# Kernel optimization log

Hardware: AMD Instinct MI355X
Metric: run time of the kernel (lower is better)

The kernel has to match this reference:

```python
import jax, jax.numpy as jnp
import numpy as np

A, D, F = 2048, 64, 12  # atoms, depth, filter_length


def _chemconv(x, conn, bond, filters):
    # x: (A, D); conn: (A, A, F); bond: (A, F, 2); filters: (D, F, D+2)
    # node_connection = conn.transpose(1,2) @ x -> (A, F, D)
    ncon = jnp.einsum('anf,nd->afd', conn, x)
    combined = jnp.concatenate([ncon, bond], axis=2)  # (A, F, D+2)
    # broadcast-multiply by filters then sum over last two dims -> (A, out_depth)
    return jnp.einsum('afc,ofc->ao', combined, filters)


def setup_inputs() -> dict:
    key = jax.random.key(0)
    k1, k2, k3, k4, k5 = jax.random.split(key, 5)
    x = jax.random.normal(k1, (A, D), dtype=jnp.float32)
    conn = jax.random.uniform(k2, (A, A, F), dtype=jnp.float32)
    bond = jax.random.normal(k3, (A, F, 2), dtype=jnp.float32)
    scale = 1.0 / D  # filters.data.normal_() * (1/in_depth)
    f0 = jax.random.normal(k4, (D, F, D + 2), dtype=jnp.float32) * scale
    f1 = jax.random.normal(k5, (D, F, D + 2), dtype=jnp.float32) * scale
    return {
        'node_property_tensor': x,
        'connectivity_tensor': conn,
        'bond_property_tensor': bond,
        'filters0': f0,
        'filters1': f1,
    }


def reference(node_property_tensor, connectivity_tensor, bond_property_tensor, filters0, filters1):
    x = node_property_tensor
    out = x
    for filt in (filters0, filters1):
        # each ChemConv layer is applied twice (same weights), per the torch code
        out = jax.nn.relu(_chemconv(out, connectivity_tensor, bond_property_tensor, filt))
        out = _chemconv(out, connectivity_tensor, bond_property_tensor, filt)
        out = out + x  # residual to the original block input
        out = jax.nn.relu(out)
    return out
```

## Files before the change

kernel.cpp:

```cpp
#include <hip/hip_runtime.h>


#define A_N 2048
#define D_N 64
#define F_N 12
#define K_TOTAL (A_N * F_N)
#define NSPLIT 32
#define KSEG (K_TOTAL / NSPLIT)
#define BK 64
#define NKB (KSEG / BK)

typedef short short8 __attribute__((ext_vector_type(8)));
typedef float f32x16 __attribute__((ext_vector_type(16)));

#define GLOAD16(ldsp, gp)                                                        \
  __builtin_amdgcn_global_load_lds(                                              \
      (const __attribute__((address_space(1))) void*)(gp),                       \
      (__attribute__((address_space(3))) void*)(ldsp), 16, 0, 0)

#define VMWAIT(n) asm volatile("s_waitcnt vmcnt(" #n ")" ::: "memory")

__device__ __forceinline__ unsigned pk_bf16(float a, float b) {
  unsigned ua = __float_as_uint(a);
  unsigned ub = __float_as_uint(b);
  ua += 0x7fffu + ((ua >> 16) & 1u);
  ub += 0x7fffu + ((ub >> 16) & 1u);
  return (ua >> 16) | (ub & 0xffff0000u);
}

__device__ __forceinline__ unsigned short bf16_1(float v) {
  unsigned u = __float_as_uint(v);
  u += 0x7fffu + ((u >> 16) & 1u);
  return (unsigned short)(u >> 16);
}

__global__ void k_prep(const float* __restrict__ x, float* __restrict__ xt,
                       const float* __restrict__ bond, const float* __restrict__ f0,
                       const float* __restrict__ f1, float* __restrict__ bt0,
                       float* __restrict__ bt1) {
  int t = threadIdx.x;
  if (blockIdx.x < 32) {
    __shared__ float ld[64][65];
    int m0 = blockIdx.x * 64;
    int r = t >> 2, cq = (t & 3) * 16;
    const float4* src = (const float4*)(x + (size_t)(m0 + r) * 64 + cq);
#pragma unroll
    for (int i = 0; i < 4; ++i) {
      float4 v = src[i];
      ld[r][cq + i * 4 + 0] = v.x;
      ld[r][cq + i * 4 + 1] = v.y;
      ld[r][cq + i * 4 + 2] = v.z;
      ld[r][cq + i * 4 + 3] = v.w;
    }
    __syncthreads();
    int c = t >> 2, ml0 = (t & 3) * 16;
    float4* dst = (float4*)(xt + (size_t)c * 2048 + m0 + ml0);
#pragma unroll
    for (int i = 0; i < 4; ++i) {
      float4 v;
      v.x = ld[ml0 + i * 4 + 0][c];
      v.y = ld[ml0 + i * 4 + 1][c];
      v.z = ld[ml0 + i * 4 + 2][c];
      v.w = ld[ml0 + i * 4 + 3][c];
      dst[i] = v;
    }
  } else {
    int b = blockIdx.x - 32;
    int a = (b & 31) * 64 + (t & 63);
    int o = (b >> 5) * 4 + (t >> 6);
    float s0 = 0.f, s1 = 0.f;
#pragma unroll
    for (int f = 0; f < F_N; ++f) {
#pragma unroll
      for (int j = 0; j < 2; ++j) {
        float bv = bond[a * 24 + f * 2 + j];
        s0 += bv * f0[o * 792 + f * 66 + 64 + j];
        s1 += bv * f1[o * 792 + f * 66 + 64 + j];
      }
    }
    bt0[o * 2048 + a] = s0;
    bt1[o * 2048 + a] = s1;
  }
}

__global__ void k_cvt(const float* __restrict__ conn, unsigned short* __restrict__ connt) {
  int t = threadIdx.x;
  int kb = blockIdx.x, ks = blockIdx.y, atile = blockIdx.z;
  const float* src = conn + (size_t)(atile * 128) * K_TOTAL + ks * KSEG + kb * 64;
  unsigned short* dst = connt + (size_t)((atile * NSPLIT + ks) * NKB + kb) * 8192;
  int r0 = t >> 3, c0 = (t & 7) * 8;
#pragma unroll
  for (int i = 0; i < 4; ++i) {
    int row = r0 + i * 32;
    const float4* s4 = (const float4*)(src + (size_t)row * K_TOTAL + c0);
    float4 a = s4[0], b = s4[1];
    uint4 p;
    p.x = pk_bf16(a.x, a.y);
    p.y = pk_bf16(a.z, a.w);
    p.z = pk_bf16(b.x, b.y);
    p.w = pk_bf16(b.z, b.w);
    *(uint4*)(dst + row * 64 + c0) = p;
  }
}

__global__ void k_g(const float* __restrict__ vt, const float* __restrict__ filt,
                    unsigned short* __restrict__ gtt) {
  __shared__ __align__(16) float WT[64][12];
  int o = blockIdx.y;
  int t = threadIdx.x;
  for (int i = t; i < 768; i += 256) {
    int d = i / 12, f = i % 12;
    WT[d][f] = filt[o * 792 + f * 66 + d];
  }
  __syncthreads();
  int n0 = blockIdx.x * 512 + t;
  float acc0[12], acc1[12];
#pragma unroll
  for (int f = 0; f < 12; ++f) { acc0[f] = 0.f; acc1[f] = 0.f; }
#pragma unroll 4
  for (int d = 0; d < 64; ++d) {
    float v0 = vt[d * 2048 + n0];
    float v1 = vt[d * 2048 + n0 + 256];
    const float4* wp = (const float4*)WT[d];
    float4 w0 = wp[0], w1 = wp[1], w2 = wp[2];
    acc0[0] += v0 * w0.x;  acc0[1] += v0 * w0.y;  acc0[2]  += v0 * w0.z;  acc0[3]  += v0 * w0.w;
    acc0[4] += v0 * w1.x;  acc0[5] += v0 * w1.y;  acc0[6]  += v0 * w1.z;  acc0[7]  += v0 * w1.w;
    acc0[8] += v0 * w2.x;  acc0[9] += v0 * w2.y;  acc0[10] += v0 * w2.z;  acc0[11] += v0 * w2.w;
    acc1[0] += v1 * w0.x;  acc1[1] += v1 * w0.y;  acc1[2]  += v1 * w0.z;  acc1[3]  += v1 * w0.w;
    acc1[4] += v1 * w1.x;  acc1[5] += v1 * w1.y;  acc1[6]  += v1 * w1.z;  acc1[7]  += v1 * w1.w;
    acc1[8] += v1 * w2.x;  acc1[9] += v1 * w2.y;  acc1[10] += v1 * w2.z;  acc1[11] += v1 * w2.w;
  }
  int kb0 = n0 * 12;
#pragma unroll
  for (int f = 0; f < F_N; ++f) {
    int k = kb0 + f;
    gtt[(size_t)(k >> 6) * 4096 + o * 64 + (k & 63)] = bf16_1(acc0[f]);
  }
  int kb1 = (n0 + 256) * 12;
#pragma unroll
  for (int f = 0; f < F_N; ++f) {
    int k = kb1 + f;
    gtt[(size_t)(k >> 6) * 4096 + o * 64 + (k & 63)] = bf16_1(acc1[f]);
  }
}

__launch_bounds__(256, 2)
__global__ void k_big(const unsigned short* __restrict__ connt,
                      const unsigned short* __restrict__ gtt, float* __restrict__ part) {
  __shared__ __align__(16) unsigned short smem[36864];
  int t = threadIdx.x, lane = t & 63, w = t >> 6;
  int atile = blockIdx.x, ks = blockIdx.y;
  const unsigned short* ct = connt + (size_t)(atile * NSPLIT + ks) * (NKB * 8192);
  const unsigned short* gs = gtt + (size_t)ks * (NKB * 4096);

  int rl = lane >> 3, sl = lane & 7;
  int cs = sl ^ rl;

  int cSrc[4], gSrc[2], cDst[4], gDst[2];
#pragma unroll
  for (int j = 0; j < 4; ++j) {
    cSrc[j] = (w * 32 + j * 8 + rl) * 64 + cs * 8;
    cDst[j] = (w * 32 + j * 8) * 64;
  }
#pragma unroll
  for (int j = 0; j < 2; ++j) {
    gSrc[j] = (w * 16 + j * 8 + rl) * 64 + cs * 8;
    gDst[j] = 8192 + (w * 16 + j * 8) * 64;
  }

  f32x16 acc0, acc1;
#pragma unroll
  for (int i = 0; i < 16; ++i) { acc0[i] = 0.f; acc1[i] = 0.f; }

  int oh = w >> 1, ah = w & 1;
  int orow = oh * 32 + (lane & 31);
  int arow = ah * 64 + (lane & 31);
  int sw = lane & 7;
  int khalf = lane >> 5;

#pragma unroll
  for (int p = 0; p < 2; ++p) {
    unsigned short* base = smem + p * 12288;
#pragma unroll
    for (int j = 0; j < 4; ++j) GLOAD16(base + cDst[j], ct + p * 8192 + cSrc[j]);
#pragma unroll
    for (int j = 0; j < 2; ++j) GLOAD16(base + gDst[j], gs + p * 4096 + gSrc[j]);
  }

#pragma unroll
  for (int kb = 0; kb < NKB; ++kb) {
    if (kb < NKB - 1) VMWAIT(6);
    else VMWAIT(0);
    __builtin_amdgcn_s_barrier();
    asm volatile("" ::: "memory");
    if (kb + 2 < NKB) {
      unsigned short* base = smem + ((kb + 2) % 3) * 12288;
#pragma unroll
      for (int j = 0; j < 4; ++j) GLOAD16(base + cDst[j], ct + (kb + 2) * 8192 + cSrc[j]);
#pragma unroll
      for (int j = 0; j < 2; ++j) GLOAD16(base + gDst[j], gs + (kb + 2) * 4096 + gSrc[j]);
    }
    const unsigned short* cb = smem + (kb % 3) * 12288;
    const unsigned short* gb = cb + 8192;
#pragma unroll
    for (int kk = 0; kk < 4; ++kk) {
      int c = kk * 2 + khalf;
      int coff = ((c ^ sw) << 3);
      short8 af = *(const short8*)(gb + orow * 64 + coff);
      short8 b0 = *(const short8*)(cb + arow * 64 + coff);
      short8 b1 = *(const short8*)(cb + (arow + 32) * 64 + coff);
      acc0 = __builtin_amdgcn_mfma_f32_32x32x16_bf16(af, b0, acc0, 0, 0, 0);
      acc1 = __builtin_amdgcn_mfma_f32_32x32x16_bf16(af, b1, acc1, 0, 0, 0);
    }
  }

  float* pp = part + (size_t)ks * (64 * 2048);
  int a0 = atile * 128 + ah * 64 + (lane & 31);
  int ob = oh * 32 + 4 * khalf;
#pragma unroll
  for (int rg = 0; rg < 16; ++rg) {
    int o = ob + (rg & 3) + 8 * (rg >> 2);
    pp[o * 2048 + a0] = acc0[rg];
    pp[o * 2048 + a0 + 32] = acc1[rg];
  }
}

__global__ void k_reduce(const float* __restrict__ part, const float* __restrict__ bt,
                         const float* __restrict__ xt, float* __restrict__ curt,
                         float* __restrict__ outp, int residual, int final_layer) {
  int i4 = blockIdx.x * 256 + threadIdx.x;
  float4 s = ((const float4*)bt)[i4];
#pragma unroll
  for (int sI = 0; sI < NSPLIT; ++sI) {
    float4 p = ((const float4*)part)[(size_t)sI * 32768 + i4];
    s.x += p.x; s.y += p.y; s.z += p.z; s.w += p.w;
  }
  if (residual) {
    float4 r = ((const float4*)xt)[i4];
    s.x += r.x; s.y += r.y; s.z += r.z; s.w += r.w;
  }
  s.x = fmaxf(s.x, 0.f); s.y = fmaxf(s.y, 0.f);
  s.z = fmaxf(s.z, 0.f); s.w = fmaxf(s.w, 0.f);
  ((float4*)curt)[i4] = s;
  if (final_layer) {
    int idx = i4 * 4;
    int o = idx >> 11, m = idx & 2047;
    outp[(m + 0) * 64 + o] = s.x;
    outp[(m + 1) * 64 + o] = s.y;
    outp[(m + 2) * 64 + o] = s.z;
    outp[(m + 3) * 64 + o] = s.w;
  }
}

extern "C" void kernel_launch(void* const* d_in, const int* in_sizes, int n_in,
                              void* d_out, int out_size, void* d_ws, size_t ws_size,
                              hipStream_t stream) {
  const float* x    = (const float*)d_in[0];
  const float* conn = (const float*)d_in[1];
  const float* bond = (const float*)d_in[2];
  const float* f0   = (const float*)d_in[3];
  const float* f1   = (const float*)d_in[4];
  float* out = (float*)d_out;

  char* ws = (char*)d_ws;
  float* xt   = (float*)(ws + 0);
  float* curt = (float*)(ws + 524288);
  float* bt0  = (float*)(ws + 1048576);
  float* bt1  = (float*)(ws + 1572864);
  unsigned short* gtt = (unsigned short*)(ws + 2097152);
  float* part = (float*)(ws + 5242880);
  unsigned short* connt = (unsigned short*)(ws + 33554432);

  k_prep<<<544, 256, 0, stream>>>(x, xt, bond, f0, f1, bt0, bt1);
  k_cvt<<<dim3(NKB, NSPLIT, 16), 256, 0, stream>>>(conn, connt);

  for (int layer = 0; layer < 4; ++layer) {
    const float* filt = (layer < 2) ? f0 : f1;
    const float* bt   = (layer < 2) ? bt0 : bt1;
    const float* vin  = (layer == 0) ? xt : curt;
    k_g<<<dim3(4, 64), 256, 0, stream>>>(vin, filt, gtt);
    k_big<<<dim3(16, NSPLIT), 256, 0, stream>>>(connt, gtt, part);
    k_reduce<<<128, 256, 0, stream>>>(part, bt, xt, curt, out, layer & 1, layer == 3);
  }
}
```

Measured before the change: 458.2 us.

## Fuse per-layer kernels into one cooperative persistent kernel with grid syncs

Merges the prep and conversion kernels into a single launch. Replaces the twelve per-layer launches (g, big GEMM, reduce) with one cooperative kernel of 512 blocks that steps through the phases using grid-wide syncs, and keeps a non-cooperative fallback. The g phase now stages its bf16 output in shared memory for coalesced writes, and the reduce phase splits the partial-sum loop across four waves. The goal is to remove launch gaps and tail effects between small kernels, at the cost of grid.sync overhead and a dependence on all 512 blocks being co-resident at two blocks per CU.

```diff
diff --git a/kernel.cpp b/kernel.cpp
--- a/kernel.cpp
+++ b/kernel.cpp
@@ -1,4 +1,7 @@
 #include <hip/hip_runtime.h>
+#include <hip/hip_cooperative_groups.h>
+
+namespace cg = cooperative_groups;
 
 
 #define A_N 2048
@@ -34,14 +37,15 @@
   return (unsigned short)(u >> 16);
 }
 
-__global__ void k_prep(const float* __restrict__ x, float* __restrict__ xt,
-                       const float* __restrict__ bond, const float* __restrict__ f0,
-                       const float* __restrict__ f1, float* __restrict__ bt0,
-                       float* __restrict__ bt1) {
-  int t = threadIdx.x;
-  if (blockIdx.x < 32) {
+__global__ void k_pre(const float* __restrict__ x, float* __restrict__ xt,
+                      const float* __restrict__ bond, const float* __restrict__ f0,
+                      const float* __restrict__ f1, float* __restrict__ bt0,
+                      float* __restrict__ bt1, const float* __restrict__ conn,
+                      unsigned short* __restrict__ connt) {
+  int t = threadIdx.x, b = blockIdx.x;
+  if (b < 32) {
     __shared__ float ld[64][65];
-    int m0 = blockIdx.x * 64;
+    int m0 = b * 64;
     int r = t >> 2, cq = (t & 3) * 16;
     const float4* src = (const float4*)(x + (size_t)(m0 + r) * 64 + cq);
 #pragma unroll
@@ -64,10 +68,10 @@
       v.w = ld[ml0 + i * 4 + 3][c];
       dst[i] = v;
     }
-  } else {
-    int b = blockIdx.x - 32;
-    int a = (b & 31) * 64 + (t & 63);
-    int o = (b >> 5) * 4 + (t >> 6);
+  } else if (b < 544) {
+    int b2 = b - 32;
+    int a = (b2 & 31) * 64 + (t & 63);
+    int o = (b2 >> 5) * 4 + (t >> 6);
     float s0 = 0.f, s1 = 0.f;
 #pragma unroll
     for (int f = 0; f < F_N; ++f) {
@@ -80,76 +84,72 @@
     }
     bt0[o * 2048 + a] = s0;
     bt1[o * 2048 + a] = s1;
-  }
-}
-
-__global__ void k_cvt(const float* __restrict__ conn, unsigned short* __restrict__ connt) {
-  int t = threadIdx.x;
-  int kb = blockIdx.x, ks = blockIdx.y, atile = blockIdx.z;
-  const float* src = conn + (size_t)(atile * 128) * K_TOTAL + ks * KSEG + kb * 64;
-  unsigned short* dst = connt + (size_t)((atile * NSPLIT + ks) * NKB + kb) * 8192;
-  int r0 = t >> 3, c0 = (t & 7) * 8;
-#pragma unroll
-  for (int i = 0; i < 4; ++i) {
-    int row = r0 + i * 32;
-    const float4* s4 = (const float4*)(src + (size_t)row * K_TOTAL + c0);
-    float4 a = s4[0], b = s4[1];
-    uint4 p;
-    p.x = pk_bf16(a.x, a.y);
-    p.y = pk_bf16(a.z, a.w);
-    p.z = pk_bf16(b.x, b.y);
-    p.w = pk_bf16(b.z, b.w);
-    *(uint4*)(dst + row * 64 + c0) = p;
-  }
-}
-
-__global__ void k_g(const float* __restrict__ vt, const float* __restrict__ filt,
-                    unsigned short* __restrict__ gtt) {
-  __shared__ __align__(16) float WT[64][12];
-  int o = blockIdx.y;
-  int t = threadIdx.x;
+  } else {
+    int i = b - 544;
+    int atile = i / 384;
+    int r2 = i % 384;
+    int ks = r2 / 12, kb = r2 % 12;
+    const float* src = conn + (size_t)(atile * 128) * K_TOTAL + ks * KSEG + kb * 64;
+    unsigned short* dst = connt + (size_t)((atile * NSPLIT + ks) * NKB + kb) * 8192;
+    int r0 = t >> 3, c0 = (t & 7) * 8;
+#pragma unroll
+    for (int q = 0; q < 4; ++q) {
+      int row = r0 + q * 32;
+      const float4* s4 = (const float4*)(src + (size_t)row * K_TOTAL + c0);
+      float4 a = s4[0], bb = s4[1];
+      uint4 p;
+      p.x = pk_bf16(a.x, a.y);
+      p.y = pk_bf16(a.z, a.w);
+      p.z = pk_bf16(bb.x, bb.y);
+      p.w = pk_bf16(bb.z, bb.w);
+      *(uint4*)(dst + row * 64 + c0) = p;
+    }
+  }
+}
+
+__device__ __forceinline__ void phase_g(unsigned short* smem, int bid, int t,
+                                        const float* __restrict__ vin,
+                                        const float* __restrict__ filt,
+                                        unsigned short* __restrict__ gtt) {
+  float* WT = (float*)smem;
+  unsigned short* sg = smem + 8192;
+  int o = bid >> 3, bx = bid & 7;
   for (int i = t; i < 768; i += 256) {
     int d = i / 12, f = i % 12;
-    WT[d][f] = filt[o * 792 + f * 66 + d];
+    WT[d * 12 + f] = filt[o * 792 + f * 66 + d];
   }
   __syncthreads();
-  int n0 = blockIdx.x * 512 + t;
-  float acc0[12], acc1[12];
-#pragma unroll
-  for (int f = 0; f < 12; ++f) { acc0[f] = 0.f; acc1[f] = 0.f; }
+  int n0 = bx * 256 + t;
+  float acc[12];
+#pragma unroll
+  for (int f = 0; f < 12; ++f) acc[f] = 0.f;
 #pragma unroll 4
   for (int d = 0; d < 64; ++d) {
-    float v0 = vt[d * 2048 + n0];
-    float v1 = vt[d * 2048 + n0 + 256];
-    const float4* wp = (const float4*)WT[d];
+    float v = vin[d * 2048 + n0];
+    const float4* wp = (const float4*)(WT + d * 12);
     float4 w0 = wp[0], w1 = wp[1], w2 = wp[2];
-    acc0[0] += v0 * w0.x;  acc0[1] += v0 * w0.y;  acc0[2]  += v0 * w0.z;  acc0[3]  += v0 * w0.w;
-    acc0[4] += v0 * w1.x;  acc0[5] += v0 * w1.y;  acc0[6]  += v0 * w1.z;  acc0[7]  += v0 * w1.w;
-    acc0[8] += v0 * w2.x;  acc0[9] += v0 * w2.y;  acc0[10] += v0 * w2.z;  acc0[11] += v0 * w2.w;
-    acc1[0] += v1 * w0.x;  acc1[1] += v1 * w0.y;  acc1[2]  += v1 * w0.z;  acc1[3]  += v1 * w0.w;
-    acc1[4] += v1 * w1.x;  acc1[5] += v1 * w1.y;  acc1[6]  += v1 * w1.z;  acc1[7]  += v1 * w1.w;
-    acc1[8] += v1 * w2.x;  acc1[9] += v1 * w2.y;  acc1[10] += v1 * w2.z;  acc1[11] += v1 * w2.w;
-  }
-  int kb0 = n0 * 12;
-#pragma unroll
-  for (int f = 0; f < F_N; ++f) {
-    int k = kb0 + f;
-    gtt[(size_t)(k >> 6) * 4096 + o * 64 + (k & 63)] = bf16_1(acc0[f]);
-  }
-  int kb1 = (n0 + 256) * 12;
-#pragma unroll
-  for (int f = 0; f < F_N; ++f) {
-    int k = kb1 + f;
-    gtt[(size_t)(k >> 6) * 4096 + o * 64 + (k & 63)] = bf16_1(acc1[f]);
-  }
-}
-
-__launch_bounds__(256, 2)
-__global__ void k_big(const unsigned short* __restrict__ connt,
-                      const unsigned short* __restrict__ gtt, float* __restrict__ part) {
-  __shared__ __align__(16) unsigned short smem[36864];
-  int t = threadIdx.x, lane = t & 63, w = t >> 6;
-  int atile = blockIdx.x, ks = blockIdx.y;
+    acc[0] += v * w0.x;  acc[1] += v * w0.y;  acc[2]  += v * w0.z;  acc[3]  += v * w0.w;
+    acc[4] += v * w1.x;  acc[5] += v * w1.y;  acc[6]  += v * w1.z;  acc[7]  += v * w1.w;
+    acc[8] += v * w2.x;  acc[9] += v * w2.y;  acc[10] += v * w2.z;  acc[11] += v * w2.w;
+  }
+#pragma unroll
+  for (int f = 0; f < 12; ++f) sg[t * 12 + f] = bf16_1(acc[f]);
+  __syncthreads();
+  unsigned short* gbase = gtt + (size_t)(bx * 48) * 4096 + o * 64;
+#pragma unroll
+  for (int j = 0; j < 2; ++j) {
+    int m = t + j * 256;
+    if (m < 384)
+      *(uint4*)(gbase + (size_t)(m >> 3) * 4096 + (m & 7) * 8) = *(const uint4*)(sg + m * 8);
+  }
+}
+
+__device__ __forceinline__ void phase_big(unsigned short* smem, int bid, int t,
+                                          const unsigned short* __restrict__ connt,
+                                          const unsigned short* __restrict__ gtt,
+                                          float* __restrict__ part) {
+  int lane = t & 63, w = t >> 6;
+  int atile = bid & 15, ks = bid >> 4;
   const unsigned short* ct = connt + (size_t)(atile * NSPLIT + ks) * (NKB * 8192);
   const unsigned short* gs = gtt + (size_t)ks * (NKB * 4096);
 
@@ -177,6 +177,8 @@
   int arow = ah * 64 + (lane & 31);
   int sw = lane & 7;
   int khalf = lane >> 5;
+
+  VMWAIT(0);
 
 #pragma unroll
   for (int p = 0; p < 2; ++p) {
@@ -225,31 +227,93 @@
   }
 }
 
-__global__ void k_reduce(const float* __restrict__ part, const float* __restrict__ bt,
-                         const float* __restrict__ xt, float* __restrict__ curt,
-                         float* __restrict__ outp, int residual, int final_layer) {
-  int i4 = blockIdx.x * 256 + threadIdx.x;
-  float4 s = ((const float4*)bt)[i4];
-#pragma unroll
-  for (int sI = 0; sI < NSPLIT; ++sI) {
-    float4 p = ((const float4*)part)[(size_t)sI * 32768 + i4];
+__device__ __forceinline__ void phase_red(unsigned short* smem, int bid, int t,
+                                          const float* __restrict__ part,
+                                          const float* __restrict__ bt,
+                                          const float* __restrict__ xt,
+                                          float* __restrict__ curt,
+                                          float* __restrict__ outp,
+                                          int residual, int final_layer) {
+  float4* rbuf = (float4*)smem;
+  int i4 = bid * 64 + (t & 63);
+  int quar = t >> 6;
+  int sbase = quar * 8;
+  float4 s = {0.f, 0.f, 0.f, 0.f};
+#pragma unroll
+  for (int k = 0; k < 8; ++k) {
+    float4 p = ((const float4*)part)[(size_t)(sbase + k) * 32768 + i4];
     s.x += p.x; s.y += p.y; s.z += p.z; s.w += p.w;
   }
-  if (residual) {
-    float4 r = ((const float4*)xt)[i4];
-    s.x += r.x; s.y += r.y; s.z += r.z; s.w += r.w;
-  }
-  s.x = fmaxf(s.x, 0.f); s.y = fmaxf(s.y, 0.f);
-  s.z = fmaxf(s.z, 0.f); s.w = fmaxf(s.w, 0.f);
-  ((float4*)curt)[i4] = s;
-  if (final_layer) {
-    int idx = i4 * 4;
-    int o = idx >> 11, m = idx & 2047;
-    outp[(m + 0) * 64 + o] = s.x;
-    outp[(m + 1) * 64 + o] = s.y;
-    outp[(m + 2) * 64 + o] = s.z;
-    outp[(m + 3) * 64 + o] = s.w;
-  }
+  if (quar) rbuf[(quar - 1) * 64 + (t & 63)] = s;
+  __syncthreads();
+  if (!quar) {
+    float4 a = rbuf[t], b2 = rbuf[64 + t], c2 = rbuf[128 + t];
+    float4 b = ((const float4*)bt)[i4];
+    s.x += a.x + b2.x + c2.x + b.x;
+    s.y += a.y + b2.y + c2.y + b.y;
+    s.z += a.z + b2.z + c2.z + b.z;
+    s.w += a.w + b2.w + c2.w + b.w;
+    if (residual) {
+      float4 rr = ((const float4*)xt)[i4];
+      s.x += rr.x; s.y += rr.y; s.z += rr.z; s.w += rr.w;
+    }
+    s.x = fmaxf(s.x, 0.f); s.y = fmaxf(s.y, 0.f);
+    s.z = fmaxf(s.z, 0.f); s.w = fmaxf(s.w, 0.f);
+    ((float4*)curt)[i4] = s;
+    if (final_layer) {
+      int idx = i4 * 4;
+      int o = idx >> 11, m = idx & 2047;
+      outp[(m + 0) * 64 + o] = s.x;
+      outp[(m + 1) * 64 + o] = s.y;
+      outp[(m + 2) * 64 + o] = s.z;
+      outp[(m + 3) * 64 + o] = s.w;
+    }
+  }
+}
+
+__launch_bounds__(256, 2)
+__global__ void k_mega(const unsigned short* __restrict__ connt,
+                       const float* __restrict__ f0, const float* __restrict__ f1,
+                       const float* __restrict__ xt, const float* __restrict__ bt0,
+                       const float* __restrict__ bt1, unsigned short* __restrict__ gtt,
+                       float* __restrict__ part, float* __restrict__ curt,
+                       float* __restrict__ outp) {
+  cg::grid_group grid = cg::this_grid();
+  __shared__ __align__(16) unsigned short smem[36864];
+  int t = threadIdx.x, bid = blockIdx.x;
+#pragma unroll 1
+  for (int layer = 0; layer < 4; ++layer) {
+    const float* filt = (layer < 2) ? f0 : f1;
+    const float* bt   = (layer < 2) ? bt0 : bt1;
+    const float* vin  = (layer == 0) ? xt : curt;
+    phase_g(smem, bid, t, vin, filt, gtt);
+    grid.sync();
+    phase_big(smem, bid, t, connt, gtt, part);
+    grid.sync();
+    phase_red(smem, bid, t, part, bt, xt, curt, outp, layer & 1, layer == 3);
+    if (layer < 3) grid.sync();
+  }
+}
+
+__global__ void k_g_f(const float* __restrict__ vin, const float* __restrict__ filt,
+                      unsigned short* __restrict__ gtt) {
+  __shared__ __align__(16) unsigned short smem[11264];
+  phase_g(smem, blockIdx.x, threadIdx.x, vin, filt, gtt);
+}
+
+__launch_bounds__(256, 2)
+__global__ void k_big_f(const unsigned short* __restrict__ connt,
+                        const unsigned short* __restrict__ gtt,
+                        float* __restrict__ part) {
+  __shared__ __align__(16) unsigned short smem[36864];
+  phase_big(smem, blockIdx.x, threadIdx.x, connt, gtt, part);
+}
+
+__global__ void k_red_f(const float* __restrict__ part, const float* __restrict__ bt,
+                        const float* __restrict__ xt, float* __restrict__ curt,
+                        float* __restrict__ outp, int residual, int final_layer) {
+  __shared__ __align__(16) unsigned short smem[1536];
+  phase_red(smem, blockIdx.x, threadIdx.x, part, bt, xt, curt, outp, residual, final_layer);
 }
 
 extern "C" void kernel_launch(void* const* d_in, const int* in_sizes, int n_in,
@@ -271,15 +335,39 @@
   float* part = (float*)(ws + 5242880);
   unsigned short* connt = (unsigned short*)(ws + 33554432);
 
-  k_prep<<<544, 256, 0, stream>>>(x, xt, bond, f0, f1, bt0, bt1);
-  k_cvt<<<dim3(NKB, NSPLIT, 16), 256, 0, stream>>>(conn, connt);
-
-  for (int layer = 0; layer < 4; ++layer) {
-    const float* filt = (layer < 2) ? f0 : f1;
-    const float* bt   = (layer < 2) ? bt0 : bt1;
-    const float* vin  = (layer == 0) ? xt : curt;
-    k_g<<<dim3(4, 64), 256, 0, stream>>>(vin, filt, gtt);
-    k_big<<<dim3(16, NSPLIT), 256, 0, stream>>>(connt, gtt, part);
-    k_reduce<<<128, 256, 0, stream>>>(part, bt, xt, curt, out, layer & 1, layer == 3);
-  }
-}
+  k_pre<<<6688, 256, 0, stream>>>(x, xt, bond, f0, f1, bt0, bt1, conn, connt);
+
+  static int coop = -1;
+  if (coop < 0) {
+    int dev = 0, v = 0;
+    if (hipGetDevice(&dev) == hipSuccess &&
+        hipDeviceGetAttribute(&v, hipDeviceAttributeCooperativeLaunch, dev) == hipSuccess)
+      coop = v ? 1 : 0;
+    else
+      coop = 0;
+  }
+
+  bool done = false;
+  if (coop) {
+    const unsigned short* a_connt = connt;
+    const float *a_f0 = f0, *a_f1 = f1, *a_xt = xt, *a_bt0 = bt0, *a_bt1 = bt1;
+    unsigned short* a_gtt = gtt;
+    float *a_part = part, *a_curt = curt, *a_out = out;
+    void* args[10] = {&a_connt, &a_f0, &a_f1, &a_xt, &a_bt0,
+                      &a_bt1, &a_gtt, &a_part, &a_curt, &a_out};
+    hipError_t e = hipLaunchCooperativeKernel((const void*)k_mega, dim3(512), dim3(256),
+                                              args, 0, stream);
+    if (e == hipSuccess) done = true;
+  }
+
+  if (!done) {
+    for (int layer = 0; layer < 4; ++layer) {
+      const float* filt = (layer < 2) ? f0 : f1;
+      const float* bt   = (layer < 2) ? bt0 : bt1;
+      const float* vin  = (layer == 0) ? xt : curt;
+      k_g_f<<<512, 256, 0, stream>>>(vin, filt, gtt);
+      k_big_f<<<512, 256, 0, stream>>>(connt, gtt, part);
+      k_red_f<<<512, 256, 0, stream>>>(part, bt, xt, curt, out, layer & 1, layer == 3);
+    }
+  }
+}
```

New measurement: 1.189 ms. 160% more time.

## Fuse split-K reduction into filter projection and merge prep with conversion

Applied to the files above, without the earlier changes.

The prep and conn-to-bf16 conversion kernels become one launch. Each layer's split-K reduction (bias, residual, ReLU) is folded into the next layer's filter-projection kernel, k_rg, which computes gtt straight from the partial sums and stages the result in LDS for coalesced stores. A separate reduction runs only after the last layer, now splitting the 32 partials across four wavefronts and combining them in LDS. This cuts kernel launches and intermediate round-trips, but each k_rg block re-reduces the partials for its atom tile across four output groups, multiplying partial-sum reads, and runs only 128 blocks.

```diff
diff --git a/kernel.cpp b/kernel.cpp
--- a/kernel.cpp
+++ b/kernel.cpp
@@ -34,14 +34,15 @@
   return (unsigned short)(u >> 16);
 }
 
-__global__ void k_prep(const float* __restrict__ x, float* __restrict__ xt,
-                       const float* __restrict__ bond, const float* __restrict__ f0,
-                       const float* __restrict__ f1, float* __restrict__ bt0,
-                       float* __restrict__ bt1) {
-  int t = threadIdx.x;
-  if (blockIdx.x < 32) {
+__global__ void k_pre(const float* __restrict__ x, float* __restrict__ xt,
+                      const float* __restrict__ bond, const float* __restrict__ f0,
+                      const float* __restrict__ f1, float* __restrict__ bt0,
+                      float* __restrict__ bt1, const float* __restrict__ conn,
+                      unsigned short* __restrict__ connt) {
+  int t = threadIdx.x, b = blockIdx.x;
+  if (b < 32) {
     __shared__ float ld[64][65];
-    int m0 = blockIdx.x * 64;
+    int m0 = b * 64;
     int r = t >> 2, cq = (t & 3) * 16;
     const float4* src = (const float4*)(x + (size_t)(m0 + r) * 64 + cq);
 #pragma unroll
@@ -64,10 +65,10 @@
       v.w = ld[ml0 + i * 4 + 3][c];
       dst[i] = v;
     }
-  } else {
-    int b = blockIdx.x - 32;
-    int a = (b & 31) * 64 + (t & 63);
-    int o = (b >> 5) * 4 + (t >> 6);
+  } else if (b < 544) {
+    int b2 = b - 32;
+    int a = (b2 & 31) * 64 + (t & 63);
+    int o = (b2 >> 5) * 4 + (t >> 6);
     float s0 = 0.f, s1 = 0.f;
 #pragma unroll
     for (int f = 0; f < F_N; ++f) {
@@ -80,67 +81,117 @@
     }
     bt0[o * 2048 + a] = s0;
     bt1[o * 2048 + a] = s1;
-  }
-}
-
-__global__ void k_cvt(const float* __restrict__ conn, unsigned short* __restrict__ connt) {
+  } else {
+    int i = b - 544;
+    int atile = i / 384;
+    int r2 = i % 384;
+    int ks = r2 / 12, kb = r2 % 12;
+    const float* src = conn + (size_t)(atile * 128) * K_TOTAL + ks * KSEG + kb * 64;
+    unsigned short* dst = connt + (size_t)((atile * NSPLIT + ks) * NKB + kb) * 8192;
+    int r0 = t >> 3, c0 = (t & 7) * 8;
+#pragma unroll
+    for (int q = 0; q < 4; ++q) {
+      int row = r0 + q * 32;
+      const float4* s4 = (const float4*)(src + (size_t)row * K_TOTAL + c0);
+      float4 a = s4[0], bb = s4[1];
+      uint4 p;
+      p.x = pk_bf16(a.x, a.y);
+      p.y = pk_bf16(a.z, a.w);
+      p.z = pk_bf16(bb.x, bb.y);
+      p.w = pk_bf16(bb.z, bb.w);
+      *(uint4*)(dst + row * 64 + c0) = p;
+    }
+  }
+}
+
+__global__ void k_rg(const float* __restrict__ part, const float* __restrict__ xt,
+                     const float* __restrict__ bt, const float* __restrict__ filt,
+                     unsigned short* __restrict__ gtt, int mode, int residual) {
+  __shared__ __align__(16) float vin[64][66];
+  __shared__ __align__(16) unsigned short sg[16][768];
   int t = threadIdx.x;
-  int kb = blockIdx.x, ks = blockIdx.y, atile = blockIdx.z;
-  const float* src = conn + (size_t)(atile * 128) * K_TOTAL + ks * KSEG + kb * 64;
-  unsigned short* dst = connt + (size_t)((atile * NSPLIT + ks) * NKB + kb) * 8192;
-  int r0 = t >> 3, c0 = (t & 7) * 8;
-#pragma unroll
-  for (int i = 0; i < 4; ++i) {
-    int row = r0 + i * 32;
-    const float4* s4 = (const float4*)(src + (size_t)row * K_TOTAL + c0);
-    float4 a = s4[0], b = s4[1];
-    uint4 p;
-    p.x = pk_bf16(a.x, a.y);
-    p.y = pk_bf16(a.z, a.w);
-    p.z = pk_bf16(b.x, b.y);
-    p.w = pk_bf16(b.z, b.w);
-    *(uint4*)(dst + row * 64 + c0) = p;
-  }
-}
-
-__global__ void k_g(const float* __restrict__ vt, const float* __restrict__ filt,
-                    unsigned short* __restrict__ gtt) {
-  __shared__ __align__(16) float WT[64][12];
-  int o = blockIdx.y;
-  int t = threadIdx.x;
-  for (int i = t; i < 768; i += 256) {
-    int d = i / 12, f = i % 12;
-    WT[d][f] = filt[o * 792 + f * 66 + d];
+  int oq = blockIdx.x, ks = blockIdx.y;
+  int a0 = ks * 64;
+
+  {
+    int d = t >> 2, j4 = (t & 3) * 16;
+    float4 s[4];
+    if (mode == 0) {
+      const float4* xp = (const float4*)(xt + (size_t)d * 2048 + a0 + j4);
+#pragma unroll
+      for (int i = 0; i < 4; ++i) s[i] = xp[i];
+    } else {
+#pragma unroll
+      for (int i = 0; i < 4; ++i) s[i] = make_float4(0.f, 0.f, 0.f, 0.f);
+#pragma unroll 4
+      for (int sp = 0; sp < NSPLIT; ++sp) {
+        const float4* pp =
+            (const float4*)(part + (size_t)sp * 131072 + (size_t)d * 2048 + a0 + j4);
+#pragma unroll
+        for (int i = 0; i < 4; ++i) {
+          float4 p = pp[i];
+          s[i].x += p.x; s[i].y += p.y; s[i].z += p.z; s[i].w += p.w;
+        }
+      }
+      const float4* bp = (const float4*)(bt + (size_t)d * 2048 + a0 + j4);
+#pragma unroll
+      for (int i = 0; i < 4; ++i) {
+        float4 p = bp[i];
+        s[i].x += p.x; s[i].y += p.y; s[i].z += p.z; s[i].w += p.w;
+      }
+      if (residual) {
+        const float4* xp = (const float4*)(xt + (size_t)d * 2048 + a0 + j4);
+#pragma unroll
+        for (int i = 0; i < 4; ++i) {
+          float4 p = xp[i];
+          s[i].x += p.x; s[i].y += p.y; s[i].z += p.z; s[i].w += p.w;
+        }
+      }
+#pragma unroll
+      for (int i = 0; i < 4; ++i) {
+        s[i].x = fmaxf(s[i].x, 0.f); s[i].y = fmaxf(s[i].y, 0.f);
+        s[i].z = fmaxf(s[i].z, 0.f); s[i].w = fmaxf(s[i].w, 0.f);
+      }
+    }
+    const float* sf = (const float*)s;
+#pragma unroll
+    for (int i = 0; i < 16; ++i) vin[j4 + i][d] = sf[i];
   }
   __syncthreads();
-  int n0 = blockIdx.x * 512 + t;
-  float acc0[12], acc1[12];
-#pragma unroll
-  for (int f = 0; f < 12; ++f) { acc0[f] = 0.f; acc1[f] = 0.f; }
-#pragma unroll 4
-  for (int d = 0; d < 64; ++d) {
-    float v0 = vt[d * 2048 + n0];
-    float v1 = vt[d * 2048 + n0 + 256];
-    const float4* wp = (const float4*)WT[d];
-    float4 w0 = wp[0], w1 = wp[1], w2 = wp[2];
-    acc0[0] += v0 * w0.x;  acc0[1] += v0 * w0.y;  acc0[2]  += v0 * w0.z;  acc0[3]  += v0 * w0.w;
-    acc0[4] += v0 * w1.x;  acc0[5] += v0 * w1.y;  acc0[6]  += v0 * w1.z;  acc0[7]  += v0 * w1.w;
-    acc0[8] += v0 * w2.x;  acc0[9] += v0 * w2.y;  acc0[10] += v0 * w2.z;  acc0[11] += v0 * w2.w;
-    acc1[0] += v1 * w0.x;  acc1[1] += v1 * w0.y;  acc1[2]  += v1 * w0.z;  acc1[3]  += v1 * w0.w;
-    acc1[4] += v1 * w1.x;  acc1[5] += v1 * w1.y;  acc1[6]  += v1 * w1.z;  acc1[7]  += v1 * w1.w;
-    acc1[8] += v1 * w2.x;  acc1[9] += v1 * w2.y;  acc1[10] += v1 * w2.z;  acc1[11] += v1 * w2.w;
-  }
-  int kb0 = n0 * 12;
-#pragma unroll
-  for (int f = 0; f < F_N; ++f) {
-    int k = kb0 + f;
-    gtt[(size_t)(k >> 6) * 4096 + o * 64 + (k & 63)] = bf16_1(acc0[f]);
-  }
-  int kb1 = (n0 + 256) * 12;
-#pragma unroll
-  for (int f = 0; f < F_N; ++f) {
-    int k = kb1 + f;
-    gtt[(size_t)(k >> 6) * 4096 + o * 64 + (k & 63)] = bf16_1(acc1[f]);
+
+  int a = t & 63, oh = t >> 6;
+  float acc[48];
+#pragma unroll
+  for (int i = 0; i < 48; ++i) acc[i] = 0.f;
+  const float* Wb = filt + (size_t)(oq * 16 + oh * 4) * 792;
+#pragma unroll 1
+  for (int dc = 0; dc < 4; ++dc) {
+    float v[16];
+#pragma unroll
+    for (int i = 0; i < 16; ++i) v[i] = vin[a][dc * 16 + i];
+#pragma unroll
+    for (int o4 = 0; o4 < 4; ++o4) {
+#pragma unroll
+      for (int f = 0; f < 12; ++f) {
+        const float* wp = Wb + o4 * 792 + f * 66 + dc * 16;
+#pragma unroll
+        for (int i = 0; i < 16; ++i) acc[o4 * 12 + f] += v[i] * wp[i];
+      }
+    }
+  }
+#pragma unroll
+  for (int o4 = 0; o4 < 4; ++o4) {
+#pragma unroll
+    for (int f = 0; f < 12; ++f) sg[oh * 4 + o4][a * 12 + f] = bf16_1(acc[o4 * 12 + f]);
+  }
+  __syncthreads();
+
+  if (t < 192) {
+    int ql = t >> 4, ol = t & 15;
+    uint4* dst = (uint4*)(gtt + (size_t)(ks * 12 + ql) * 4096 + (oq * 16 + ol) * 64);
+    const uint4* src = (const uint4*)(&sg[ol][ql * 64]);
+#pragma unroll
+    for (int i = 0; i < 8; ++i) dst[i] = src[i];
   }
 }
 
@@ -225,30 +276,44 @@
   }
 }
 
-__global__ void k_reduce(const float* __restrict__ part, const float* __restrict__ bt,
-                         const float* __restrict__ xt, float* __restrict__ curt,
-                         float* __restrict__ outp, int residual, int final_layer) {
-  int i4 = blockIdx.x * 256 + threadIdx.x;
-  float4 s = ((const float4*)bt)[i4];
-#pragma unroll
-  for (int sI = 0; sI < NSPLIT; ++sI) {
-    float4 p = ((const float4*)part)[(size_t)sI * 32768 + i4];
+__global__ void k_red(const float* __restrict__ part, const float* __restrict__ bt,
+                      const float* __restrict__ xt, float* __restrict__ curt,
+                      float* __restrict__ outp, int residual, int final_layer) {
+  __shared__ __align__(16) float4 rbuf[192];
+  int t = threadIdx.x, bid = blockIdx.x;
+  int i4 = bid * 64 + (t & 63);
+  int quar = t >> 6;
+  int sbase = quar * 8;
+  float4 s = {0.f, 0.f, 0.f, 0.f};
+#pragma unroll
+  for (int k = 0; k < 8; ++k) {
+    float4 p = ((const float4*)part)[(size_t)(sbase + k) * 32768 + i4];
     s.x += p.x; s.y += p.y; s.z += p.z; s.w += p.w;
   }
-  if (residual) {
-    float4 r = ((const float4*)xt)[i4];
-    s.x += r.x; s.y += r.y; s.z += r.z; s.w += r.w;
-  }
-  s.x = fmaxf(s.x, 0.f); s.y = fmaxf(s.y, 0.f);
-  s.z = fmaxf(s.z, 0.f); s.w = fmaxf(s.w, 0.f);
-  ((float4*)curt)[i4] = s;
-  if (final_layer) {
-    int idx = i4 * 4;
-    int o = idx >> 11, m = idx & 2047;
-    outp[(m + 0) * 64 + o] = s.x;
-    outp[(m + 1) * 64 + o] = s.y;
-    outp[(m + 2) * 64 + o] = s.z;
-    outp[(m + 3) * 64 + o] = s.w;
+  if (quar) rbuf[(quar - 1) * 64 + (t & 63)] = s;
+  __syncthreads();
+  if (!quar) {
+    float4 a = rbuf[t], b2 = rbuf[64 + t], c2 = rbuf[128 + t];
+    float4 b = ((const float4*)bt)[i4];
+    s.x += a.x + b2.x + c2.x + b.x;
+    s.y += a.y + b2.y + c2.y + b.y;
+    s.z += a.z + b2.z + c2.z + b.z;
+    s.w += a.w + b2.w + c2.w + b.w;
+    if (residual) {
+      float4 rr = ((const float4*)xt)[i4];
+      s.x += rr.x; s.y += rr.y; s.z += rr.z; s.w += rr.w;
+    }
+    s.x = fmaxf(s.x, 0.f); s.y = fmaxf(s.y, 0.f);
+    s.z = fmaxf(s.z, 0.f); s.w = fmaxf(s.w, 0.f);
+    ((float4*)curt)[i4] = s;
+    if (final_layer) {
+      int idx = i4 * 4;
+      int o = idx >> 11, m = idx & 2047;
+      outp[(m + 0) * 64 + o] = s.x;
+      outp[(m + 1) * 64 + o] = s.y;
+      outp[(m + 2) * 64 + o] = s.z;
+      outp[(m + 3) * 64 + o] = s.w;
+    }
   }
 }
 
@@ -271,15 +336,15 @@
   float* part = (float*)(ws + 5242880);
   unsigned short* connt = (unsigned short*)(ws + 33554432);
 
-  k_prep<<<544, 256, 0, stream>>>(x, xt, bond, f0, f1, bt0, bt1);
-  k_cvt<<<dim3(NKB, NSPLIT, 16), 256, 0, stream>>>(conn, connt);
-
-  for (int layer = 0; layer < 4; ++layer) {
-    const float* filt = (layer < 2) ? f0 : f1;
-    const float* bt   = (layer < 2) ? bt0 : bt1;
-    const float* vin  = (layer == 0) ? xt : curt;
-    k_g<<<dim3(4, 64), 256, 0, stream>>>(vin, filt, gtt);
-    k_big<<<dim3(16, NSPLIT), 256, 0, stream>>>(connt, gtt, part);
-    k_reduce<<<128, 256, 0, stream>>>(part, bt, xt, curt, out, layer & 1, layer == 3);
-  }
-}
+  k_pre<<<6688, 256, 0, stream>>>(x, xt, bond, f0, f1, bt0, bt1, conn, connt);
+
+  k_rg<<<dim3(4, NSPLIT), 256, 0, stream>>>(part, xt, bt0, f0, gtt, 0, 0);
+  k_big<<<dim3(16, NSPLIT), 256, 0, stream>>>(connt, gtt, part);
+  k_rg<<<dim3(4, NSPLIT), 256, 0, stream>>>(part, xt, bt0, f0, gtt, 1, 0);
+  k_big<<<dim3(16, NSPLIT), 256, 0, stream>>>(connt, gtt, part);
+  k_rg<<<dim3(4, NSPLIT), 256, 0, stream>>>(part, xt, bt0, f1, gtt, 1, 1);
+  k_big<<<dim3(16, NSPLIT), 256, 0, stream>>>(connt, gtt, part);
+  k_rg<<<dim3(4, NSPLIT), 256, 0, stream>>>(part, xt, bt1, f1, gtt, 1, 0);
+  k_big<<<dim3(16, NSPLIT), 256, 0, stream>>>(connt, gtt, part);
+  k_red<<<512, 256, 0, stream>>>(part, bt1, xt, curt, out, 1, 1);
+}
```

After: 548.7 us. +19.8%, slower.
